# Kernel optimization log

Measured on AMD Instinct MI355X. Metric: run time of the kernel, lower is better.

The kernel has to match this reference:

```python
import jax, jax.numpy as jnp
import numpy as np

B, C, H, W, K = 16, 512, 64, 64, 64  # K = external-attention latent dim (self.k = 64)


def setup_inputs() -> dict:
    key = jax.random.key(0)
    ks = jax.random.split(key, 5)
    x = jax.random.normal(ks[0], (B, C, H, W), dtype=jnp.float32)
    # conv1: Conv2d(c, c, 1) with bias; init normal(0, sqrt(2/(1*1*out_channels)))
    conv1_w = jax.random.normal(ks[1], (C, C), dtype=jnp.float32) * np.float32(np.sqrt(2.0 / C))
    conv1_b = jnp.zeros((C,), dtype=jnp.float32)
    # linear_0: Conv1d(c, k, 1, bias=False); init normal(0, sqrt(2/out_channels))
    lin0_w = jax.random.normal(ks[2], (K, C), dtype=jnp.float32) * np.float32(np.sqrt(2.0 / K))
    # linear_1: Conv1d(k, c, 1, bias=False)
    lin1_w = jax.random.normal(ks[3], (C, K), dtype=jnp.float32) * np.float32(np.sqrt(2.0 / C))
    # conv2: Conv2d(c, c, 1, bias=False)
    conv2_w = jax.random.normal(ks[4], (C, C), dtype=jnp.float32) * np.float32(np.sqrt(2.0 / C))
    return {"x": x, "conv1_w": conv1_w, "conv1_b": conv1_b,
            "lin0_w": lin0_w, "lin1_w": lin1_w, "conv2_w": conv2_w}


def reference(x, conv1_w, conv1_b, lin0_w, lin1_w, conv2_w):
    b, c, h, w = x.shape
    n = h * w
    idn = x
    # conv1: 1x1 conv == per-pixel GEMM
    y = jnp.einsum('oc,bchw->bohw', conv1_w, x) + conv1_b[None, :, None, None]
    y = y.reshape(b, c, n)
    # external attention: linear_0 -> softmax over tokens -> L1 renorm over latent dim
    attn = jnp.einsum('kc,bcn->bkn', lin0_w, y)          # (b, K, n)
    attn = jax.nn.softmax(attn, axis=-1)
    attn = attn / (1e-9 + attn.sum(axis=1, keepdims=True))
    y = jnp.einsum('ck,bkn->bcn', lin1_w, attn)          # (b, c, n)
    # rank: view(-1, c) row-major (as torch .view does), per-row topk threshold,
    # scale below-threshold by 0.75 and the rest by 1.25; output is detached
    # (torch.tensor(pred, requires_grad=False)) -> stop_gradient
    top_k = c // 2
    flat = y.reshape(-1, c)                               # (b*n, c) row-major chunks
    thr = jax.lax.top_k(flat, top_k)[0][:, -1:]           # k-th largest per row
    scaled = jnp.where(flat < thr, 0.75 * flat, 1.25 * flat)
    yr = jax.lax.stop_gradient(scaled).reshape(b, c, h, w)
    # conv2: 1x1 conv no bias + ReLU, residual add, final ReLU
    out = jax.nn.relu(jnp.einsum('oc,bchw->bohw', conv2_w, yr))
    return jax.nn.relu(out + idn)
```

## Files before the change

### kernel.cpp

```cpp
#include <hip/hip_runtime.h>
#include <stdint.h>

typedef unsigned short u16;
typedef unsigned int u32;
using short8 = __attribute__((ext_vector_type(8))) short;
using f32x4  = __attribute__((ext_vector_type(4))) float;

#define BDIM 16
#define CDIM 512
#define KLAT 64
#define NTOK 4096

__device__ __forceinline__ u16 f2bf(float x) {
  union { float f; u32 u; } a; a.f = x;
  u32 r = a.u + 0x7FFFu + ((a.u >> 16) & 1u);
  return (u16)(r >> 16);
}
__device__ __forceinline__ u32 pack2(float a, float b) {
  return (u32)f2bf(a) | ((u32)f2bf(b) << 16);
}
__device__ __forceinline__ u32 f2key(float x) {
  u32 u = __float_as_uint(x);
  return (u & 0x80000000u) ? ~u : (u | 0x80000000u);
}
__device__ __forceinline__ float keyscale(u32 k_, u32 thr) {
  u32 u = (k_ & 0x80000000u) ? (k_ & 0x7FFFFFFFu) : ~k_;
  float v = __uint_as_float(u);
  return (k_ < thr) ? 0.75f * v : 1.25f * v;
}

__global__ __launch_bounds__(256) void k_setup(
    const float* __restrict__ conv1_w, const float* __restrict__ conv1_b,
    const float* __restrict__ lin0_w,  const float* __restrict__ lin1_w,
    const float* __restrict__ conv2_w,
    u16* __restrict__ w0bf, float* __restrict__ b0,
    u16* __restrict__ lin1bf, u16* __restrict__ cwbf)
{
  const int bid = blockIdx.x;
  const int t = threadIdx.x;
  if (bid < 128) {
    const int kb = bid & 15, cb = bid >> 4;
    const int lane = t & 63;
    int k = kb * 4 + (t >> 6);
    k = __builtin_amdgcn_readfirstlane(k);
    const int c = cb * 64 + lane;
    float acc = 0.f;
    const float* l0 = lin0_w + (size_t)k * CDIM;
    const float* cw = conv1_w + c;
#pragma unroll 4
    for (int o = 0; o < CDIM; ++o)
      acc = fmaf(l0[o], cw[(size_t)o * CDIM], acc);
    w0bf[k * CDIM + c] = f2bf(acc);
  } else if (bid == 128) {
    if (t < KLAT) {
      float acc = 0.f;
      for (int c = 0; c < CDIM; ++c) acc = fmaf(lin0_w[t * CDIM + c], conv1_b[c], acc);
      b0[t] = acc;
    }
  } else if (bid < 193) {
    const int b2 = bid - 129;
    const float4* src = (const float4*)conv2_w;
#pragma unroll
    for (int i = 0; i < 4; ++i) {
      int idx = (b2 * 256 + t) + i * 16384;
      float4 v = src[idx];
      uint2 o;
      o.x = pack2(v.x, v.y);
      o.y = pack2(v.z, v.w);
      *(uint2*)(cwbf + (size_t)idx * 4) = o;
    }
  } else {
    const int b2 = bid - 193;
#pragma unroll
    for (int i = 0; i < 4; ++i) {
      int g = b2 * 1024 + i * 256 + t;
      float4 v0 = *(const float4*)(lin1_w + (size_t)g * 8);
      float4 v1 = *(const float4*)(lin1_w + (size_t)g * 8 + 4);
      uint4 o;
      o.x = pack2(v0.x, v0.y); o.y = pack2(v0.z, v0.w);
      o.z = pack2(v1.x, v1.y); o.w = pack2(v1.z, v1.w);
      *(uint4*)(lin1bf + (size_t)g * 8) = o;
    }
  }
}

__global__ __launch_bounds__(256) void k_xpose(
    const float* __restrict__ x, u16* __restrict__ xbt)
{
  __shared__ float tile[32 * 512];
  const int n0 = blockIdx.x * 512, c0 = blockIdx.y * 32, b = blockIdx.z;
  const int t = threadIdx.x;
#pragma unroll
  for (int i = 0; i < 16; ++i) {
    int f4 = t + i * 256;
    int row = f4 >> 7, col4 = f4 & 127;
    float4 v = *(const float4*)(x + ((size_t)(b * CDIM + c0 + row)) * NTOK + n0 + col4 * 4);
    int phys4 = (col4 + row + (row >> 3)) & 127;
    *(float4*)&tile[row * 512 + phys4 * 4] = v;
  }
  __syncthreads();
#pragma unroll
  for (int i = 0; i < 8; ++i) {
    int nr = (t >> 2) + i * 64;
    int cs = (t & 3) * 8;
    float w[8];
#pragma unroll
    for (int j = 0; j < 8; ++j) {
      int row = cs + j;
      int phys4 = ((nr >> 2) + row + (row >> 3)) & 127;
      w[j] = tile[row * 512 + phys4 * 4 + (nr & 3)];
    }
    uint4 o;
    o.x = pack2(w[0], w[1]); o.y = pack2(w[2], w[3]);
    o.z = pack2(w[4], w[5]); o.w = pack2(w[6], w[7]);
    *(uint4*)(xbt + ((size_t)(b * NTOK + n0 + nr)) * CDIM + c0 + cs) = o;
  }
}

__global__ __launch_bounds__(256) void k_logits(
    const u16* __restrict__ w0bf, const u16* __restrict__ xbt,
    const float* __restrict__ b0, float* __restrict__ logits)
{
  __shared__ u16 As[64 * 72];
  __shared__ u16 Bs[128 * 72];
  const int nb = blockIdx.x, b = blockIdx.y;
  const int t = threadIdx.x;
  const int wv = t >> 6, lane = t & 63;
  const int quad = lane >> 4, l15 = lane & 15;
  f32x4 acc[4][2];
#pragma unroll
  for (int mi = 0; mi < 4; ++mi)
#pragma unroll
    for (int ni = 0; ni < 2; ++ni) acc[mi][ni] = (f32x4){0.f, 0.f, 0.f, 0.f};

  for (int kc = 0; kc < 8; ++kc) {
#pragma unroll
    for (int i = 0; i < 2; ++i) {
      int ch = t + i * 256;
      int row = ch >> 3, col = (ch & 7) * 8;
      uint4 a = *(const uint4*)(w0bf + (size_t)row * CDIM + kc * 64 + col);
      *(uint4*)&As[row * 72 + col] = a;
    }
#pragma unroll
    for (int i = 0; i < 4; ++i) {
      int ch = t + i * 256;
      int row = ch >> 3, col = (ch & 7) * 8;
      uint4 bb = *(const uint4*)(xbt + ((size_t)(b * NTOK + nb * 128 + row)) * CDIM + kc * 64 + col);
      *(uint4*)&Bs[row * 72 + col] = bb;
    }
    __syncthreads();
#pragma unroll
    for (int kk = 0; kk < 2; ++kk) {
      short8 af[4], bf_[2];
#pragma unroll
      for (int mi = 0; mi < 4; ++mi)
        af[mi] = *(short8*)&As[(mi * 16 + l15) * 72 + kk * 32 + quad * 8];
#pragma unroll
      for (int ni = 0; ni < 2; ++ni)
        bf_[ni] = *(short8*)&Bs[(wv * 32 + ni * 16 + l15) * 72 + kk * 32 + quad * 8];
#pragma unroll
      for (int mi = 0; mi < 4; ++mi)
#pragma unroll
        for (int ni = 0; ni < 2; ++ni)
          acc[mi][ni] = __builtin_amdgcn_mfma_f32_16x16x32_bf16(
              af[mi], bf_[ni], acc[mi][ni], 0, 0, 0);
    }
    __syncthreads();
  }
#pragma unroll
  for (int mi = 0; mi < 4; ++mi) {
#pragma unroll
    for (int ni = 0; ni < 2; ++ni) {
#pragma unroll
      for (int r = 0; r < 4; ++r) {
        int row = mi * 16 + quad * 4 + r;
        int col = nb * 128 + wv * 32 + ni * 16 + l15;
        logits[((size_t)(b * KLAT + row)) * NTOK + col] = acc[mi][ni][r] + b0[row];
      }
    }
  }
}

__global__ __launch_bounds__(256) void k_softmax(float* __restrict__ attn)
{
  __shared__ float red[4], red2[4];
  const int t = threadIdx.x;
  float* p = attn + (size_t)blockIdx.x * NTOK;
  float4 v[4];
#pragma unroll
  for (int i = 0; i < 4; ++i) v[i] = ((float4*)p)[t + i * 256];
  float m = v[0].x;
#pragma unroll
  for (int i = 0; i < 4; ++i)
    m = fmaxf(m, fmaxf(fmaxf(v[i].x, v[i].y), fmaxf(v[i].z, v[i].w)));
#pragma unroll
  for (int o = 1; o < 64; o <<= 1) m = fmaxf(m, __shfl_xor(m, o));
  const int wv = t >> 6, lane = t & 63;
  if (lane == 0) red[wv] = m;
  __syncthreads();
  m = fmaxf(fmaxf(red[0], red[1]), fmaxf(red[2], red[3]));
  float s = 0.f;
#pragma unroll
  for (int i = 0; i < 4; ++i) {
    v[i].x = __expf(v[i].x - m); s += v[i].x;
    v[i].y = __expf(v[i].y - m); s += v[i].y;
    v[i].z = __expf(v[i].z - m); s += v[i].z;
    v[i].w = __expf(v[i].w - m); s += v[i].w;
  }
#pragma unroll
  for (int o = 1; o < 64; o <<= 1) s += __shfl_xor(s, o);
  if (lane == 0) red2[wv] = s;
  __syncthreads();
  s = red2[0] + red2[1] + red2[2] + red2[3];
  const float inv = 1.f / s;
#pragma unroll
  for (int i = 0; i < 4; ++i) {
    v[i].x *= inv; v[i].y *= inv; v[i].z *= inv; v[i].w *= inv;
    ((float4*)p)[t + i * 256] = v[i];
  }
}

__global__ __launch_bounds__(256) void k_attnT(
    const float* __restrict__ attn, u16* __restrict__ attnT)
{
  __shared__ float tile[64 * 256];
  __shared__ float inv_[256];
  const int n0 = blockIdx.x * 256, b = blockIdx.y;
  const int t = threadIdx.x;
#pragma unroll
  for (int i = 0; i < 16; ++i) {
    int f4 = t + i * 256;
    int row = f4 >> 6, col4 = f4 & 63;
    float4 v = *(const float4*)(attn + ((size_t)(b * KLAT + row)) * NTOK + n0 + col4 * 4);
    int phys4 = (col4 + row + (row >> 3)) & 63;
    *(float4*)&tile[row * 256 + phys4 * 4] = v;
  }
  __syncthreads();
  {
    int n4 = t >> 2, sub = t & 3;
    float s = 0.f;
#pragma unroll
    for (int k = 0; k < 64; ++k) {
      int phys4 = (n4 + k + (k >> 3)) & 63;
      s += tile[k * 256 + phys4 * 4 + sub];
    }
    inv_[t] = 1.f / (1e-9f + s);
  }
  __syncthreads();
#pragma unroll
  for (int i = 0; i < 8; ++i) {
    int nr = (t >> 3) + i * 32;
    int cs = (t & 7) * 8;
    float sc = inv_[nr];
    float w[8];
#pragma unroll
    for (int j = 0; j < 8; ++j) {
      int row = cs + j;
      int phys4 = ((nr >> 2) + row + (row >> 3)) & 63;
      w[j] = tile[row * 256 + phys4 * 4 + (nr & 3)] * sc;
    }
    uint4 o;
    o.x = pack2(w[0], w[1]); o.y = pack2(w[2], w[3]);
    o.z = pack2(w[4], w[5]); o.w = pack2(w[6], w[7]);
    *(uint4*)(attnT + ((size_t)(b * NTOK + n0 + nr)) * KLAT + cs) = o;
  }
}

__global__ __launch_bounds__(512) void k_lin1rank(
    const u16* __restrict__ lin1bf, const u16* __restrict__ attnT,
    u16* __restrict__ yrt)
{
  __shared__ float tile[32 * 512];
  const int n0 = blockIdx.x * 512, c0 = blockIdx.y * 32, b = blockIdx.z;
  const int t = threadIdx.x;
  const int wv = t >> 6, lane = t & 63;
  const int quad = lane >> 4, l15 = lane & 15;

  short8 af[2][2], bfr[4][2];
#pragma unroll
  for (int mi = 0; mi < 2; ++mi)
#pragma unroll
    for (int kk = 0; kk < 2; ++kk)
      af[mi][kk] = *(const short8*)(lin1bf +
          (size_t)(c0 + mi * 16 + l15) * KLAT + kk * 32 + quad * 8);
#pragma unroll
  for (int ni = 0; ni < 4; ++ni)
#pragma unroll
    for (int kk = 0; kk < 2; ++kk)
      bfr[ni][kk] = *(const short8*)(attnT +
          ((size_t)(b * NTOK + n0 + wv * 64 + ni * 16 + l15)) * KLAT + kk * 32 + quad * 8);
  f32x4 acc[2][4];
#pragma unroll
  for (int mi = 0; mi < 2; ++mi)
#pragma unroll
    for (int ni = 0; ni < 4; ++ni) acc[mi][ni] = (f32x4){0.f, 0.f, 0.f, 0.f};
#pragma unroll
  for (int kk = 0; kk < 2; ++kk)
#pragma unroll
    for (int mi = 0; mi < 2; ++mi)
#pragma unroll
      for (int ni = 0; ni < 4; ++ni)
        acc[mi][ni] = __builtin_amdgcn_mfma_f32_16x16x32_bf16(
            af[mi][kk], bfr[ni][kk], acc[mi][ni], 0, 0, 0);
#pragma unroll
  for (int mi = 0; mi < 2; ++mi) {
#pragma unroll
    for (int ni = 0; ni < 4; ++ni) {
#pragma unroll
      for (int r = 0; r < 4; ++r) {
        int row = mi * 16 + quad * 4 + r;
        int col = wv * 64 + ni * 16 + l15;
        int phys4 = ((col >> 2) + row + (row >> 3)) & 127;
        tile[row * 512 + phys4 * 4 + (col & 3)] = acc[mi][ni][r];
      }
    }
  }
  __syncthreads();

#pragma unroll
  for (int r = 0; r < 4; ++r) {
    const int row = wv * 4 + r;
    const int rot = row + (row >> 3);
    const int c4a = (lane + rot) & 127;
    const int c4b = (64 + lane + rot) & 127;
    float* pa = &tile[row * 512 + c4a * 4];
    float* pb = &tile[row * 512 + c4b * 4];
    float4 va = *(const float4*)pa;
    float4 vb = *(const float4*)pb;
    u32 key[8];
    key[0] = f2key(va.x); key[1] = f2key(va.y);
    key[2] = f2key(va.z); key[3] = f2key(va.w);
    key[4] = f2key(vb.x); key[5] = f2key(vb.y);
    key[6] = f2key(vb.z); key[7] = f2key(vb.w);
    u32 kmin = key[0], kmax = key[0];
#pragma unroll
    for (int j = 1; j < 8; ++j) {
      kmin = key[j] < kmin ? key[j] : kmin;
      kmax = key[j] > kmax ? key[j] : kmax;
    }
#pragma unroll
    for (int o = 1; o < 64; o <<= 1) {
      u32 a_ = __shfl_xor(kmin, o), b_ = __shfl_xor(kmax, o);
      kmin = a_ < kmin ? a_ : kmin;
      kmax = b_ > kmax ? b_ : kmax;
    }
    u32 lo = kmin, hi = kmax;
    u32 thr;
    if (lo >= hi) thr = lo;
    else for (;;) {
      u32 d = hi - lo;
      u32 mid = lo + (d >> 1) + (d & 1u);
      int cnt = 0;
#pragma unroll
      for (int j = 0; j < 8; ++j)
        cnt += (int)__popcll(__ballot(key[j] >= mid));
      if (cnt == 256) { thr = mid; break; }
      if (cnt > 256) lo = mid; else hi = mid - 1u;
      if (lo >= hi) { thr = lo; break; }
    }
    float4 oa, ob;
    oa.x = keyscale(key[0], thr); oa.y = keyscale(key[1], thr);
    oa.z = keyscale(key[2], thr); oa.w = keyscale(key[3], thr);
    ob.x = keyscale(key[4], thr); ob.y = keyscale(key[5], thr);
    ob.z = keyscale(key[6], thr); ob.w = keyscale(key[7], thr);
    *(float4*)pa = oa;
    *(float4*)pb = ob;
  }
  __syncthreads();

#pragma unroll
  for (int i = 0; i < 4; ++i) {
    int nr = (t >> 2) + i * 128;
    int cs = (t & 3) * 8;
    float w[8];
#pragma unroll
    for (int j = 0; j < 8; ++j) {
      int row = cs + j;
      int phys4 = ((nr >> 2) + row + (row >> 3)) & 127;
      w[j] = tile[row * 512 + phys4 * 4 + (nr & 3)];
    }
    uint4 o;
    o.x = pack2(w[0], w[1]); o.y = pack2(w[2], w[3]);
    o.z = pack2(w[4], w[5]); o.w = pack2(w[6], w[7]);
    *(uint4*)(yrt + ((size_t)(b * NTOK + n0 + nr)) * CDIM + c0 + cs) = o;
  }
}

__global__ __launch_bounds__(256) void k_conv2(
    const u16* __restrict__ cwbf, const u16* __restrict__ yrt,
    const float* __restrict__ x, float* __restrict__ out)
{
  __shared__ u16 As[128 * 72];
  __shared__ u16 Bs[128 * 72];
  const int nb = blockIdx.x, mb = blockIdx.y, b = blockIdx.z;
  const int t = threadIdx.x;
  const int wv = t >> 6, lane = t & 63;
  const int wm = wv >> 1, wn = wv & 1;
  const int quad = lane >> 4, l15 = lane & 15;
  f32x4 acc[4][4];
#pragma unroll
  for (int mi = 0; mi < 4; ++mi)
#pragma unroll
    for (int ni = 0; ni < 4; ++ni) acc[mi][ni] = (f32x4){0.f, 0.f, 0.f, 0.f};

  for (int kc = 0; kc < 8; ++kc) {
#pragma unroll
    for (int i = 0; i < 4; ++i) {
      int ch = t + i * 256;
      int row = ch >> 3, col = (ch & 7) * 8;
      uint4 a = *(const uint4*)(cwbf + ((size_t)(mb * 128 + row)) * CDIM + kc * 64 + col);
      *(uint4*)&As[row * 72 + col] = a;
      uint4 bb = *(const uint4*)(yrt + ((size_t)(b * NTOK + nb * 128 + row)) * CDIM + kc * 64 + col);
      *(uint4*)&Bs[row * 72 + col] = bb;
    }
    __syncthreads();
#pragma unroll
    for (int kk = 0; kk < 2; ++kk) {
      short8 af[4], bf_[4];
#pragma unroll
      for (int mi = 0; mi < 4; ++mi)
        af[mi] = *(short8*)&As[(wm * 64 + mi * 16 + l15) * 72 + kk * 32 + quad * 8];
#pragma unroll
      for (int ni = 0; ni < 4; ++ni)
        bf_[ni] = *(short8*)&Bs[(wn * 64 + ni * 16 + l15) * 72 + kk * 32 + quad * 8];
#pragma unroll
      for (int mi = 0; mi < 4; ++mi)
#pragma unroll
        for (int ni = 0; ni < 4; ++ni)
          acc[mi][ni] = __builtin_amdgcn_mfma_f32_16x16x32_bf16(
              af[mi], bf_[ni], acc[mi][ni], 0, 0, 0);
    }
    __syncthreads();
  }
#pragma unroll
  for (int mi = 0; mi < 4; ++mi) {
#pragma unroll
    for (int ni = 0; ni < 4; ++ni) {
#pragma unroll
      for (int r = 0; r < 4; ++r) {
        int row = mb * 128 + wm * 64 + mi * 16 + quad * 4 + r;
        int col = nb * 128 + wn * 64 + ni * 16 + l15;
        size_t off = ((size_t)(b * CDIM + row)) * NTOK + col;
        float g = fmaxf(acc[mi][ni][r], 0.f) + x[off];
        out[off] = fmaxf(g, 0.f);
      }
    }
  }
}

extern "C" void kernel_launch(void* const* d_in, const int* in_sizes, int n_in,
                              void* d_out, int out_size, void* d_ws, size_t ws_size,
                              hipStream_t stream)
{
  const float* x       = (const float*)d_in[0];
  const float* conv1_w = (const float*)d_in[1];
  const float* conv1_b = (const float*)d_in[2];
  const float* lin0_w  = (const float*)d_in[3];
  const float* lin1_w  = (const float*)d_in[4];
  const float* conv2_w = (const float*)d_in[5];
  float* out = (float*)d_out;

  char* ws = (char*)d_ws;
  float* attn  = (float*)ws;
  u16*   xbt   = (u16*)(ws + 16777216);
  u16*   yrt   = xbt;
  u16*   attnT = (u16*)d_out;
  char*  wsm   = ws + 16777216 + 67108864;
  u16*   w0bf  = (u16*)wsm;
  float* b0    = (float*)(wsm + 131072);
  u16*   lin1bf= (u16*)(wsm + 131328);
  u16*   cwbf  = (u16*)(wsm + 262400);

  k_setup   <<<197, 256, 0, stream>>>(conv1_w, conv1_b, lin0_w, lin1_w, conv2_w,
                                      w0bf, b0, lin1bf, cwbf);
  k_xpose   <<<dim3(8, 16, 16), 256, 0, stream>>>(x, xbt);
  k_logits  <<<dim3(32, 16), 256, 0, stream>>>(w0bf, xbt, b0, attn);
  k_softmax <<<1024, 256, 0, stream>>>(attn);
  k_attnT   <<<dim3(16, 16), 256, 0, stream>>>(attn, attnT);
  k_lin1rank<<<dim3(8, 16, 16), 512, 0, stream>>>(lin1bf, attnT, yrt);
  k_conv2   <<<dim3(32, 4, 16), 256, 0, stream>>>(cwbf, yrt, x, out);
}
```

Baseline: 486.3 us.

## Fuse x transpose into logits GEMM and use direct global-to-LDS loads in conv2

Removes the separate k_xpose kernel and has k_logits read fp32 x directly into a swizzled LDS tile, converting to bf16 while building MFMA fragments. This drops a full write and re-read of a bf16 transposed copy of x. Separately, conv2 now stages its A and B tiles with global_load_lds into XOR-swizzled unpadded LDS, replacing the register round trip. The costs are a larger fp32 LDS tile and per-element scalar LDS reads plus conversions in the logits inner loop.

```diff
diff --git a/kernel.cpp b/kernel.cpp
--- a/kernel.cpp
+++ b/kernel.cpp
@@ -27,6 +27,11 @@
   u32 u = (k_ & 0x80000000u) ? (k_ & 0x7FFFFFFFu) : ~k_;
   float v = __uint_as_float(u);
   return (k_ < thr) ? 0.75f * v : 1.25f * v;
+}
+__device__ __forceinline__ void gload_lds16(const void* g, void* l) {
+  __builtin_amdgcn_global_load_lds(
+      (const __attribute__((address_space(1))) unsigned int*)g,
+      (__attribute__((address_space(3))) unsigned int*)l, 16, 0, 0);
 }
 
 __global__ __launch_bounds__(256) void k_setup(
@@ -84,45 +89,12 @@
   }
 }
 
-__global__ __launch_bounds__(256) void k_xpose(
-    const float* __restrict__ x, u16* __restrict__ xbt)
-{
-  __shared__ float tile[32 * 512];
-  const int n0 = blockIdx.x * 512, c0 = blockIdx.y * 32, b = blockIdx.z;
-  const int t = threadIdx.x;
-#pragma unroll
-  for (int i = 0; i < 16; ++i) {
-    int f4 = t + i * 256;
-    int row = f4 >> 7, col4 = f4 & 127;
-    float4 v = *(const float4*)(x + ((size_t)(b * CDIM + c0 + row)) * NTOK + n0 + col4 * 4);
-    int phys4 = (col4 + row + (row >> 3)) & 127;
-    *(float4*)&tile[row * 512 + phys4 * 4] = v;
-  }
-  __syncthreads();
-#pragma unroll
-  for (int i = 0; i < 8; ++i) {
-    int nr = (t >> 2) + i * 64;
-    int cs = (t & 3) * 8;
-    float w[8];
-#pragma unroll
-    for (int j = 0; j < 8; ++j) {
-      int row = cs + j;
-      int phys4 = ((nr >> 2) + row + (row >> 3)) & 127;
-      w[j] = tile[row * 512 + phys4 * 4 + (nr & 3)];
-    }
-    uint4 o;
-    o.x = pack2(w[0], w[1]); o.y = pack2(w[2], w[3]);
-    o.z = pack2(w[4], w[5]); o.w = pack2(w[6], w[7]);
-    *(uint4*)(xbt + ((size_t)(b * NTOK + n0 + nr)) * CDIM + c0 + cs) = o;
-  }
-}
-
 __global__ __launch_bounds__(256) void k_logits(
-    const u16* __restrict__ w0bf, const u16* __restrict__ xbt,
+    const u16* __restrict__ w0bf, const float* __restrict__ x,
     const float* __restrict__ b0, float* __restrict__ logits)
 {
   __shared__ u16 As[64 * 72];
-  __shared__ u16 Bs[128 * 72];
+  __shared__ float xt[64 * 128];
   const int nb = blockIdx.x, b = blockIdx.y;
   const int t = threadIdx.x;
   const int wv = t >> 6, lane = t & 63;
@@ -142,11 +114,13 @@
       *(uint4*)&As[row * 72 + col] = a;
     }
 #pragma unroll
-    for (int i = 0; i < 4; ++i) {
-      int ch = t + i * 256;
-      int row = ch >> 3, col = (ch & 7) * 8;
-      uint4 bb = *(const uint4*)(xbt + ((size_t)(b * NTOK + nb * 128 + row)) * CDIM + kc * 64 + col);
-      *(uint4*)&Bs[row * 72 + col] = bb;
+    for (int i = 0; i < 8; ++i) {
+      int f4 = t + i * 256;
+      int row = f4 >> 5, col4 = f4 & 31;
+      float4 v = *(const float4*)(x + ((size_t)(b * CDIM + kc * 64 + row)) * NTOK
+                                  + nb * 128 + col4 * 4);
+      int phys4 = (col4 + row + (row >> 3)) & 31;
+      *(float4*)&xt[row * 128 + phys4 * 4] = v;
     }
     __syncthreads();
 #pragma unroll
@@ -156,8 +130,20 @@
       for (int mi = 0; mi < 4; ++mi)
         af[mi] = *(short8*)&As[(mi * 16 + l15) * 72 + kk * 32 + quad * 8];
 #pragma unroll
-      for (int ni = 0; ni < 2; ++ni)
-        bf_[ni] = *(short8*)&Bs[(wv * 32 + ni * 16 + l15) * 72 + kk * 32 + quad * 8];
+      for (int ni = 0; ni < 2; ++ni) {
+        const int n = wv * 32 + ni * 16 + l15;
+        const int n4 = n >> 2, ns = n & 3;
+        union { u32 u[4]; short8 s; } cvt;
+#pragma unroll
+        for (int jj = 0; jj < 4; ++jj) {
+          int ca = kk * 32 + quad * 8 + jj * 2;
+          int cb2 = ca + 1;
+          float v0 = xt[ca * 128 + (((n4 + ca + (ca >> 3)) & 31) * 4) + ns];
+          float v1 = xt[cb2 * 128 + (((n4 + cb2 + (cb2 >> 3)) & 31) * 4) + ns];
+          cvt.u[jj] = pack2(v0, v1);
+        }
+        bf_[ni] = cvt.s;
+      }
 #pragma unroll
       for (int mi = 0; mi < 4; ++mi)
 #pragma unroll
@@ -390,13 +376,14 @@
     const u16* __restrict__ cwbf, const u16* __restrict__ yrt,
     const float* __restrict__ x, float* __restrict__ out)
 {
-  __shared__ u16 As[128 * 72];
-  __shared__ u16 Bs[128 * 72];
+  __shared__ __align__(16) u16 As[128 * 64];
+  __shared__ __align__(16) u16 Bs[128 * 64];
   const int nb = blockIdx.x, mb = blockIdx.y, b = blockIdx.z;
   const int t = threadIdx.x;
   const int wv = t >> 6, lane = t & 63;
   const int wm = wv >> 1, wn = wv & 1;
   const int quad = lane >> 4, l15 = lane & 15;
+  const int lrow = lane >> 3, lg = lane & 7;
   f32x4 acc[4][4];
 #pragma unroll
   for (int mi = 0; mi < 4; ++mi)
@@ -406,23 +393,30 @@
   for (int kc = 0; kc < 8; ++kc) {
 #pragma unroll
     for (int i = 0; i < 4; ++i) {
-      int ch = t + i * 256;
-      int row = ch >> 3, col = (ch & 7) * 8;
-      uint4 a = *(const uint4*)(cwbf + ((size_t)(mb * 128 + row)) * CDIM + kc * 64 + col);
-      *(uint4*)&As[row * 72 + col] = a;
-      uint4 bb = *(const uint4*)(yrt + ((size_t)(b * NTOK + nb * 128 + row)) * CDIM + kc * 64 + col);
-      *(uint4*)&Bs[row * 72 + col] = bb;
+      const int r0 = i * 32 + wv * 8;
+      const int row = r0 + lrow;
+      const int gsrc = lg ^ (row & 7);
+      const u16* ga = cwbf + ((size_t)(mb * 128 + row)) * CDIM + kc * 64 + gsrc * 8;
+      gload_lds16(ga, &As[r0 * 64]);
+      const u16* gb = yrt + ((size_t)(b * NTOK + nb * 128 + row)) * CDIM + kc * 64 + gsrc * 8;
+      gload_lds16(gb, &Bs[r0 * 64]);
     }
     __syncthreads();
 #pragma unroll
     for (int kk = 0; kk < 2; ++kk) {
       short8 af[4], bf_[4];
 #pragma unroll
-      for (int mi = 0; mi < 4; ++mi)
-        af[mi] = *(short8*)&As[(wm * 64 + mi * 16 + l15) * 72 + kk * 32 + quad * 8];
-#pragma unroll
-      for (int ni = 0; ni < 4; ++ni)
-        bf_[ni] = *(short8*)&Bs[(wn * 64 + ni * 16 + l15) * 72 + kk * 32 + quad * 8];
+      for (int mi = 0; mi < 4; ++mi) {
+        int row = wm * 64 + mi * 16 + l15;
+        int q = kk * 4 + quad;
+        af[mi] = *(short8*)&As[row * 64 + ((q ^ (row & 7)) * 8)];
+      }
+#pragma unroll
+      for (int ni = 0; ni < 4; ++ni) {
+        int row = wn * 64 + ni * 16 + l15;
+        int q = kk * 4 + quad;
+        bf_[ni] = *(short8*)&Bs[row * 64 + ((q ^ (row & 7)) * 8)];
+      }
 #pragma unroll
       for (int mi = 0; mi < 4; ++mi)
 #pragma unroll
@@ -462,8 +456,7 @@
 
   char* ws = (char*)d_ws;
   float* attn  = (float*)ws;
-  u16*   xbt   = (u16*)(ws + 16777216);
-  u16*   yrt   = xbt;
+  u16*   yrt   = (u16*)(ws + 16777216);
   u16*   attnT = (u16*)d_out;
   char*  wsm   = ws + 16777216 + 67108864;
   u16*   w0bf  = (u16*)wsm;
@@ -473,8 +466,7 @@
 
   k_setup   <<<197, 256, 0, stream>>>(conv1_w, conv1_b, lin0_w, lin1_w, conv2_w,
                                       w0bf, b0, lin1bf, cwbf);
-  k_xpose   <<<dim3(8, 16, 16), 256, 0, stream>>>(x, xbt);
-  k_logits  <<<dim3(32, 16), 256, 0, stream>>>(w0bf, xbt, b0, attn);
+  k_logits  <<<dim3(32, 16), 256, 0, stream>>>(w0bf, x, b0, attn);
   k_softmax <<<1024, 256, 0, stream>>>(attn);
   k_attnT   <<<dim3(16, 16), 256, 0, stream>>>(attn, attnT);
   k_lin1rank<<<dim3(8, 16, 16), 512, 0, stream>>>(lin1bf, attnT, yrt);
```

Result: no change. 477.3 us (-1.8%).
